# Kernel optimization log

Hardware: AMD Instinct MI355X
Metric: run time of the kernel (lower is better)

## Reference

```python
import jax, jax.numpy as jnp
import numpy as np

K = 4          # deform conv kernel size
STRIDE = 4     # deform conv stride (no padding)
EPS = 1e-5     # BatchNorm eps
SLOPE = 0.01   # LeakyReLU default negative slope


def conv2d(x, w, b, stride):
    out = jax.lax.conv_general_dilated(
        x, w, (stride, stride), 'VALID',
        dimension_numbers=('NCHW', 'OIHW', 'NCHW'))
    return out + b[None, :, None, None]


def batchnorm(x, g, b, m, v):
    inv = g / jnp.sqrt(v + EPS)
    return x * inv[None, :, None, None] + (b - m * inv)[None, :, None, None]


def leaky_relu(x):
    return jnp.where(x >= 0, x, SLOPE * x)


def deform_conv(x, offset, w, b):
    # x: [B,C,H,W], offset: [B,2*K*K,Ho,Wo] with (dy,dx) interleaved per kernel tap
    B, C, H, W = x.shape
    Ho, Wo = offset.shape[2], offset.shape[3]
    KK = K * K
    off = offset.reshape(B, KK, 2, Ho, Wo)
    kh = jnp.repeat(jnp.arange(K), K).astype(x.dtype)   # [KK] kernel row
    kw = jnp.tile(jnp.arange(K), K).astype(x.dtype)     # [KK] kernel col
    base_y = (jnp.arange(Ho) * STRIDE).astype(x.dtype)
    base_x = (jnp.arange(Wo) * STRIDE).astype(x.dtype)
    # sampling coordinates [B,KK,Ho,Wo]
    py = base_y[None, None, :, None] + kh[None, :, None, None] + off[:, :, 0]
    px = base_x[None, None, None, :] + kw[None, :, None, None] + off[:, :, 1]
    y0 = jnp.floor(py)
    x0 = jnp.floor(px)
    wy = py - y0
    wx = px - x0

    def corner(yc, xc):
        yi = yc.astype(jnp.int32)
        xi = xc.astype(jnp.int32)
        valid = (yi >= 0) & (yi < H) & (xi >= 0) & (xi < W)
        yi = jnp.clip(yi, 0, H - 1)
        xi = jnp.clip(xi, 0, W - 1)
        # per-batch gather: [B,C,KK,Ho,Wo]
        v = jax.vmap(lambda img, a, c: img[:, a, c])(x, yi, xi)
        return v * valid[:, None].astype(x.dtype)

    v00 = corner(y0, x0)
    v01 = corner(y0, x0 + 1)
    v10 = corner(y0 + 1, x0)
    v11 = corner(y0 + 1, x0 + 1)
    wy_ = wy[:, None]
    wx_ = wx[:, None]
    sampled = (v00 * (1 - wy_) * (1 - wx_) + v01 * (1 - wy_) * wx_
               + v10 * wy_ * (1 - wx_) + v11 * wy_ * wx_)  # [B,C,KK,Ho,Wo]
    out = jnp.einsum('bckhw,ock->bohw', sampled, w.reshape(w.shape[0], C, KK))
    return out + b[None, :, None, None]


def setup_inputs() -> dict:
    key = jax.random.key(0)
    ks = jax.random.split(key, 16)
    f32 = jnp.float32
    inp = {
        'x': jax.random.normal(ks[0], (64, 3, 224, 224), f32),
        'stem_w': jax.random.normal(ks[1], (96, 3, 4, 4), f32) * 0.1,
        'stem_b': jax.random.normal(ks[2], (96,), f32) * 0.05,
        'bn1_g': jax.random.uniform(ks[3], (96,), f32, 0.5, 1.5),
        'bn1_b': jax.random.normal(ks[4], (96,), f32) * 0.05,
        'bn1_m': jax.random.normal(ks[5], (96,), f32) * 0.05,
        'bn1_v': jax.random.uniform(ks[6], (96,), f32, 0.5, 1.5),
        'off_w': jax.random.normal(ks[7], (32, 96, 4, 4), f32) * 0.02,
        'off_b': jax.random.normal(ks[8], (32,), f32) * 0.02,
        'dcn_w': jax.random.normal(ks[9], (768, 96, 4, 4), f32) * 0.05,
        'dcn_b': jax.random.normal(ks[10], (768,), f32) * 0.05,
        'bn2_g': jax.random.uniform(ks[11], (768,), f32, 0.5, 1.5),
        'bn2_b': jax.random.normal(ks[12], (768,), f32) * 0.05,
        'bn2_m': jax.random.normal(ks[13], (768,), f32) * 0.05,
        'bn2_v': jax.random.uniform(ks[14], (768,), f32, 0.5, 1.5),
    }
    return inp


def reference(x, stem_w, stem_b, bn1_g, bn1_b, bn1_m, bn1_v,
              off_w, off_b, dcn_w, dcn_b, bn2_g, bn2_b, bn2_m, bn2_v):
    h = conv2d(x, stem_w, stem_b, 4)                      # [B,96,56,56]
    h = leaky_relu(batchnorm(h, bn1_g, bn1_b, bn1_m, bn1_v))
    offset = conv2d(h, off_w, off_b, 4)                   # [B,32,14,14]
    h = deform_conv(h, offset, dcn_w, dcn_b)              # [B,768,14,14]
    h = leaky_relu(batchnorm(h, bn2_g, bn2_b, bn2_m, bn2_v))
    B, C, Ho, Wo = h.shape
    return h.reshape(B, C, Ho * Wo).transpose(0, 2, 1)    # [B,196,768]
```

## Files before the change

kernel.cpp:

```cpp
#include <hip/hip_runtime.h>

#define EPS   1e-5f
#define SLOPE 0.01f

#define WS_H1   0L
#define WS_OFF  19267584L
#define WS_W1T  19668992L
#define WS_S1   19673600L
#define WS_T1   19673696L
#define WS_T2   19673792L
#define WS_SB   19674560L
#define WS_H1P  29308352L
#define WS_WTB  38942144L
#define WS_WOB  39531968L

__device__ __forceinline__ unsigned short f2bf(float f) {
    unsigned int u = __builtin_bit_cast(unsigned int, f);
    u += 0x7fffu + ((u >> 16) & 1u);
    return (unsigned short)(u >> 16);
}

typedef __attribute__((ext_vector_type(4))) unsigned short ushort4v;
typedef __attribute__((ext_vector_type(8))) short bf16x8;
typedef __attribute__((ext_vector_type(4))) float floatx4;

__global__ __launch_bounds__(256) void k0_prep(
    const float* __restrict__ stem_w, const float* __restrict__ stem_b,
    const float* __restrict__ bn1_g,  const float* __restrict__ bn1_b,
    const float* __restrict__ bn1_m,  const float* __restrict__ bn1_v,
    const float* __restrict__ off_w,  const float* __restrict__ dcn_w,
    const float* __restrict__ dcn_b,  const float* __restrict__ bn2_g,
    const float* __restrict__ bn2_b,  const float* __restrict__ bn2_m,
    const float* __restrict__ bn2_v,  float* __restrict__ ws)
{
    long i = (long)blockIdx.x * 256 + threadIdx.x;
    unsigned short* Wtb = (unsigned short*)(ws + WS_WTB);
    unsigned short* Wob = (unsigned short*)(ws + WS_WOB);
    if (i < 1179648L) {
        int oc = (int)(i / 1536), k = (int)(i % 1536);
        int kk = k / 96, c = k % 96;
        float inv2 = bn2_g[oc] * rsqrtf(bn2_v[oc] + EPS);
        Wtb[i] = f2bf(dcn_w[oc * 1536 + c * 16 + kk] * inv2);
    } else if (i < 1228800L) {
        int i2 = (int)(i - 1179648L);
        int oc = i2 / 1536, k = i2 % 1536;
        int khw = k / 96, c = k % 96;
        Wob[i2] = f2bf(off_w[oc * 1536 + c * 16 + khw]);
    } else if (i < 1233408L) {
        int i3 = (int)(i - 1228800L);
        int k = i3 / 96, c = i3 % 96;
        ws[WS_W1T + i3] = stem_w[c * 48 + k];
    } else if (i < 1233504L) {
        int c = (int)(i - 1233408L);
        ws[WS_S1 + c] = bn1_g[c] * rsqrtf(bn1_v[c] + EPS);
    } else if (i < 1233600L) {
        int c = (int)(i - 1233504L);
        float s = bn1_g[c] * rsqrtf(bn1_v[c] + EPS);
        ws[WS_T1 + c] = stem_b[c] * s + bn1_b[c] - bn1_m[c] * s;
    } else if (i < 1234368L) {
        int oc = (int)(i - 1233600L);
        float inv2 = bn2_g[oc] * rsqrtf(bn2_v[oc] + EPS);
        ws[WS_T2 + oc] = dcn_b[oc] * inv2 + bn2_b[oc] - bn2_m[oc] * inv2;
    }
}

__global__ __launch_bounds__(256) void k1_stem(
    const float* __restrict__ x, const float* __restrict__ w1t,
    const float* __restrict__ s1, const float* __restrict__ t1,
    float* __restrict__ h1, unsigned short* __restrict__ h1p)
{
    const int oy = blockIdx.x;
    const int b  = blockIdx.y;
    const int tid = threadIdx.x;

    __shared__ float xs[3 * 4 * 224];
    __shared__ float wsh[48 * 100];
    __shared__ float s1s[96], t1s[96];

    for (int i = tid; i < 2688; i += 256) {
        int ci = i / 896, r = i % 896;
        int kh = r / 224, xx = r % 224;
        xs[i] = x[((long)(b * 3 + ci) * 224 + oy * 4 + kh) * 224 + xx];
    }
    for (int i = tid; i < 4608; i += 256) {
        int k = i / 96, c = i % 96;
        wsh[k * 100 + c] = w1t[i];
    }
    if (tid < 96) { s1s[tid] = s1[tid]; t1s[tid] = t1[tid]; }
    __syncthreads();

    for (int u = tid; u < 336; u += 256) {
        int oxg = u / 24, cg = u % 24;
        float acc[4][4] = {};
#pragma unroll
        for (int ci = 0; ci < 3; ci++) {
#pragma unroll
            for (int kh = 0; kh < 4; kh++) {
                const float* xrow = &xs[(ci * 4 + kh) * 224 + oxg * 16];
                float4 xv[4], wv[4];
#pragma unroll
                for (int o = 0; o < 4; o++) xv[o] = *(const float4*)&xrow[o * 4];
#pragma unroll
                for (int kw = 0; kw < 4; kw++)
                    wv[kw] = *(const float4*)&wsh[(ci * 16 + kh * 4 + kw) * 100 + cg * 4];
#pragma unroll
                for (int kw = 0; kw < 4; kw++) {
                    const float* wf = (const float*)&wv[kw];
#pragma unroll
                    for (int o = 0; o < 4; o++) {
                        float xv_s = ((const float*)&xv[o])[kw];
#pragma unroll
                        for (int cc = 0; cc < 4; cc++)
                            acc[o][cc] += xv_s * wf[cc];
                    }
                }
            }
        }
#pragma unroll
        for (int o = 0; o < 4; o++) {
            float4 r;
            float* rp = (float*)&r;
#pragma unroll
            for (int cc = 0; cc < 4; cc++) {
                int c = cg * 4 + cc;
                float v = acc[o][cc] * s1s[c] + t1s[c];
                rp[cc] = v >= 0.f ? v : SLOPE * v;
            }
            *(float4*)&h1[((long)((b * 56 + oy) * 56) + oxg * 4 + o) * 96 + cg * 4] = r;
            ushort4v hp;
            hp.x = f2bf(rp[0]); hp.y = f2bf(rp[1]);
            hp.z = f2bf(rp[2]); hp.w = f2bf(rp[3]);
            long np = ((long)(b * 196 + (oy >> 2) * 14 + oxg) * 16 + (oy & 3) * 4 + o);
            *(ushort4v*)&h1p[np * 96 + cg * 4] = hp;
        }
    }
}

__global__ __launch_bounds__(256) void k2_mfma(
    const unsigned short* __restrict__ A,
    const unsigned short* __restrict__ Wob,
    const float* __restrict__ off_b, float* __restrict__ off)
{
    const int tid  = threadIdx.x;
    const int wave = tid >> 6;
    const int lane = tid & 63;
    const int n0   = blockIdx.x * 128;
    const int m    = lane & 15;
    const int quad = lane >> 4;

    __shared__ unsigned short sA[128 * 32];
    __shared__ unsigned short sB[32 * 32];

    const int srow  = wave * 32 + (lane >> 2);
    const int skoff = (lane & 3) * 8;
    const unsigned short* gA0 = A + (long)(n0 + srow) * 1536 + skoff;
    const unsigned short* gA1 = gA0 + 16L * 1536;
    unsigned short* lA0 = &sA[(wave * 32 +  0) * 32];
    unsigned short* lA1 = &sA[(wave * 32 + 16) * 32];
    const unsigned short* gB = Wob + (long)((wave & 1) * 16 + (lane >> 2)) * 1536 + skoff;
    unsigned short* lB = &sB[((wave & 1) * 16) * 32];

    floatx4 acc[2][2];
#pragma unroll
    for (int i = 0; i < 2; i++)
#pragma unroll
        for (int j = 0; j < 2; j++) acc[i][j] = (floatx4)0.f;

    for (int kt = 0; kt < 48; ++kt) {
        __syncthreads();
        __builtin_amdgcn_global_load_lds(
            (const __attribute__((address_space(1))) void*)gA0,
            (__attribute__((address_space(3))) void*)lA0, 16, 0, 0);
        __builtin_amdgcn_global_load_lds(
            (const __attribute__((address_space(1))) void*)gA1,
            (__attribute__((address_space(3))) void*)lA1, 16, 0, 0);
        if (wave < 2)
            __builtin_amdgcn_global_load_lds(
                (const __attribute__((address_space(1))) void*)gB,
                (__attribute__((address_space(3))) void*)lB, 16, 0, 0);
        gA0 += 32; gA1 += 32; gB += 32;
        __syncthreads();

        bf16x8 af[2], bfr[2];
#pragma unroll
        for (int i = 0; i < 2; i++)
            af[i] = *(const bf16x8*)&sA[(wave * 32 + i * 16 + m) * 32 + quad * 8];
#pragma unroll
        for (int j = 0; j < 2; j++)
            bfr[j] = *(const bf16x8*)&sB[(j * 16 + m) * 32 + quad * 8];
#pragma unroll
        for (int i = 0; i < 2; i++)
#pragma unroll
            for (int j = 0; j < 2; j++)
                acc[i][j] = __builtin_amdgcn_mfma_f32_16x16x32_bf16(
                    af[i], bfr[j], acc[i][j], 0, 0, 0);
    }

    float tb[2];
#pragma unroll
    for (int j = 0; j < 2; j++) tb[j] = off_b[j * 16 + m];
#pragma unroll
    for (int i = 0; i < 2; i++)
#pragma unroll
        for (int r = 0; r < 4; r++) {
            long n = n0 + wave * 32 + i * 16 + quad * 4 + r;
#pragma unroll
            for (int j = 0; j < 2; j++)
                off[n * 32 + j * 16 + m] = acc[i][j][r] + tb[j];
        }
}

__global__ __launch_bounds__(384) void k3_sample(
    const float* __restrict__ h1, const float* __restrict__ off,
    unsigned short* __restrict__ S)
{
    const int p = blockIdx.x;
    const int b = blockIdx.y;
    const int y = p / 14, xo = p % 14;
    const int tid = threadIdx.x;
    const int c4 = tid % 24, kk = tid / 24;
    const int kh = kk >> 2, kw = kk & 3;

    const float* ob = off + ((long)((b * 14 + y) * 14 + xo)) * 32;
    float dy = ob[kk * 2];
    float dx = ob[kk * 2 + 1];

    float py = (float)(y * 4 + kh) + dy;
    float px = (float)(xo * 4 + kw) + dx;
    float y0f = floorf(py), x0f = floorf(px);
    float wy = py - y0f, wx = px - x0f;
    int y0 = (int)y0f, x0 = (int)x0f;
    int y1 = y0 + 1,  x1 = x0 + 1;

    float my0 = (y0 >= 0 && y0 < 56) ? 1.f : 0.f;
    float my1 = (y1 >= 0 && y1 < 56) ? 1.f : 0.f;
    float mx0 = (x0 >= 0 && x0 < 56) ? 1.f : 0.f;
    float mx1 = (x1 >= 0 && x1 < 56) ? 1.f : 0.f;
    int y0c = min(max(y0, 0), 55), y1c = min(max(y1, 0), 55);
    int x0c = min(max(x0, 0), 55), x1c = min(max(x1, 0), 55);

    const float* hb = h1 + (long)b * 56 * 56 * 96 + c4 * 4;
    float4 v00 = *(const float4*)&hb[(y0c * 56 + x0c) * 96];
    float4 v01 = *(const float4*)&hb[(y0c * 56 + x1c) * 96];
    float4 v10 = *(const float4*)&hb[(y1c * 56 + x0c) * 96];
    float4 v11 = *(const float4*)&hb[(y1c * 56 + x1c) * 96];

    float w00 = my0 * mx0 * (1.f - wy) * (1.f - wx);
    float w01 = my0 * mx1 * (1.f - wy) * wx;
    float w10 = my1 * mx0 * wy * (1.f - wx);
    float w11 = my1 * mx1 * wy * wx;

    ushort4v rr;
    rr.x = f2bf(v00.x * w00 + v01.x * w01 + v10.x * w10 + v11.x * w11);
    rr.y = f2bf(v00.y * w00 + v01.y * w01 + v10.y * w10 + v11.y * w11);
    rr.z = f2bf(v00.z * w00 + v01.z * w01 + v10.z * w10 + v11.z * w11);
    rr.w = f2bf(v00.w * w00 + v01.w * w01 + v10.w * w10 + v11.w * w11);

    long n = (long)b * 196 + p;
    *(ushort4v*)&S[n * 1536 + kk * 96 + c4 * 4] = rr;
}

__global__ __launch_bounds__(256) void k4_gemm_mfma(
    const unsigned short* __restrict__ S,
    const unsigned short* __restrict__ Wtb,
    const float* __restrict__ t2, float* __restrict__ out)
{
    const int tid  = threadIdx.x;
    const int wave = tid >> 6;
    const int lane = tid & 63;
    const int oc0 = blockIdx.x * 128;
    const int n0  = blockIdx.y * 128;
    const int wr  = wave >> 1, wc = wave & 1;
    const int m    = lane & 15;
    const int quad = lane >> 4;

    __shared__ unsigned short sA[128 * 32];
    __shared__ unsigned short sB[128 * 32];

    const int srow  = wave * 32 + (lane >> 2);
    const int skoff = (lane & 3) * 8;
    const unsigned short* gA0 = S   + (long)(n0  + srow) * 1536 + skoff;
    const unsigned short* gA1 = gA0 + 16L * 1536;
    const unsigned short* gB0 = Wtb + (long)(oc0 + srow) * 1536 + skoff;
    const unsigned short* gB1 = gB0 + 16L * 1536;
    unsigned short* lA0 = &sA[(wave * 32 +  0) * 32];
    unsigned short* lA1 = &sA[(wave * 32 + 16) * 32];
    unsigned short* lB0 = &sB[(wave * 32 +  0) * 32];
    unsigned short* lB1 = &sB[(wave * 32 + 16) * 32];

    floatx4 acc[4][4];
#pragma unroll
    for (int i = 0; i < 4; i++)
#pragma unroll
        for (int j = 0; j < 4; j++) acc[i][j] = (floatx4)0.f;

    for (int kt = 0; kt < 48; ++kt) {
        __syncthreads();
        __builtin_amdgcn_global_load_lds(
            (const __attribute__((address_space(1))) void*)gA0,
            (__attribute__((address_space(3))) void*)lA0, 16, 0, 0);
        __builtin_amdgcn_global_load_lds(
            (const __attribute__((address_space(1))) void*)gA1,
            (__attribute__((address_space(3))) void*)lA1, 16, 0, 0);
        __builtin_amdgcn_global_load_lds(
            (const __attribute__((address_space(1))) void*)gB0,
            (__attribute__((address_space(3))) void*)lB0, 16, 0, 0);
        __builtin_amdgcn_global_load_lds(
            (const __attribute__((address_space(1))) void*)gB1,
            (__attribute__((address_space(3))) void*)lB1, 16, 0, 0);
        gA0 += 32; gA1 += 32; gB0 += 32; gB1 += 32;
        __syncthreads();

        bf16x8 af[4], bf[4];
#pragma unroll
        for (int i = 0; i < 4; i++)
            af[i] = *(const bf16x8*)&sA[(wr * 64 + i * 16 + m) * 32 + quad * 8];
#pragma unroll
        for (int j = 0; j < 4; j++)
            bf[j] = *(const bf16x8*)&sB[(wc * 64 + j * 16 + m) * 32 + quad * 8];
#pragma unroll
        for (int i = 0; i < 4; i++)
#pragma unroll
            for (int j = 0; j < 4; j++)
                acc[i][j] = __builtin_amdgcn_mfma_f32_16x16x32_bf16(
                    af[i], bf[j], acc[i][j], 0, 0, 0);
    }

    float tb[4];
#pragma unroll
    for (int j = 0; j < 4; j++) tb[j] = t2[oc0 + wc * 64 + j * 16 + m];
#pragma unroll
    for (int i = 0; i < 4; i++) {
#pragma unroll
        for (int r = 0; r < 4; r++) {
            long n = n0 + wr * 64 + i * 16 + quad * 4 + r;
            float* orow = out + n * 768 + oc0 + wc * 64 + m;
#pragma unroll
            for (int j = 0; j < 4; j++) {
                float v = acc[i][j][r] + tb[j];
                orow[j * 16] = v >= 0.f ? v : SLOPE * v;
            }
        }
    }
}

extern "C" void kernel_launch(void* const* d_in, const int* in_sizes, int n_in,
                              void* d_out, int out_size, void* d_ws, size_t ws_size,
                              hipStream_t stream)
{
    const float* x      = (const float*)d_in[0];
    const float* stem_w = (const float*)d_in[1];
    const float* stem_b = (const float*)d_in[2];
    const float* bn1_g  = (const float*)d_in[3];
    const float* bn1_b  = (const float*)d_in[4];
    const float* bn1_m  = (const float*)d_in[5];
    const float* bn1_v  = (const float*)d_in[6];
    const float* off_w  = (const float*)d_in[7];
    const float* off_b  = (const float*)d_in[8];
    const float* dcn_w  = (const float*)d_in[9];
    const float* dcn_b  = (const float*)d_in[10];
    const float* bn2_g  = (const float*)d_in[11];
    const float* bn2_b  = (const float*)d_in[12];
    const float* bn2_m  = (const float*)d_in[13];
    const float* bn2_v  = (const float*)d_in[14];

    float* ws  = (float*)d_ws;
    float* out = (float*)d_out;

    float* h1  = ws + WS_H1;
    float* off = ws + WS_OFF;
    float* w1t = ws + WS_W1T;
    float* s1  = ws + WS_S1;
    float* t1  = ws + WS_T1;
    float* t2  = ws + WS_T2;
    unsigned short* Sb  = (unsigned short*)(ws + WS_SB);
    unsigned short* h1p = (unsigned short*)(ws + WS_H1P);
    unsigned short* Wtb = (unsigned short*)(ws + WS_WTB);
    unsigned short* Wob = (unsigned short*)(ws + WS_WOB);

    k0_prep<<<4823, 256, 0, stream>>>(stem_w, stem_b, bn1_g, bn1_b, bn1_m, bn1_v,
                                      off_w, dcn_w, dcn_b, bn2_g, bn2_b, bn2_m,
                                      bn2_v, ws);
    k1_stem<<<dim3(56, 64), 256, 0, stream>>>(x, w1t, s1, t1, h1, h1p);
    k2_mfma<<<98, 256, 0, stream>>>(h1p, Wob, off_b, off);
    k3_sample<<<dim3(196, 64), 384, 0, stream>>>(h1, off, Sb);
    k4_gemm_mfma<<<dim3(6, 98), 256, 0, stream>>>(Sb, Wtb, t2, out);
}
```

Baseline: 262.4 us.

## Store stem activations once in bf16 and gather patches directly in offset conv

The stem kernel now writes a single bf16 NHWC activation instead of both an fp32 copy and a separate patch-ordered bf16 copy. The offset-conv GEMM computes patch addresses on the fly from the NHWC layout, and the bilinear sampler reads bf16 values, converts them to float and interpolates. The stem block size is raised to 384 so each thread handles one work item without a second loop pass. This cuts stem write traffic and halves sampler gather bytes, at the cost of sampling from bf16-rounded activations and less contiguous loads in the offset GEMM.

After: 252.7 us. -3.7%, faster.

```diff
diff --git a/kernel.cpp b/kernel.cpp
--- a/kernel.cpp
+++ b/kernel.cpp
@@ -3,21 +3,24 @@
 #define EPS   1e-5f
 #define SLOPE 0.01f
 
-#define WS_H1   0L
-#define WS_OFF  19267584L
-#define WS_W1T  19668992L
-#define WS_S1   19673600L
-#define WS_T1   19673696L
-#define WS_T2   19673792L
-#define WS_SB   19674560L
-#define WS_H1P  29308352L
-#define WS_WTB  38942144L
-#define WS_WOB  39531968L
+#define WS_H1B  0L
+#define WS_OFF  9633792L
+#define WS_W1T  10035200L
+#define WS_S1   10039808L
+#define WS_T1   10039904L
+#define WS_T2   10040000L
+#define WS_SB   10040768L
+#define WS_WTB  19674560L
+#define WS_WOB  20264384L
 
 __device__ __forceinline__ unsigned short f2bf(float f) {
     unsigned int u = __builtin_bit_cast(unsigned int, f);
     u += 0x7fffu + ((u >> 16) & 1u);
     return (unsigned short)(u >> 16);
+}
+__device__ __forceinline__ float bf2f(unsigned short u) {
+    unsigned int t = ((unsigned int)u) << 16;
+    return __builtin_bit_cast(float, t);
 }
 
 typedef __attribute__((ext_vector_type(4))) unsigned short ushort4v;
@@ -64,10 +67,10 @@
     }
 }
 
-__global__ __launch_bounds__(256) void k1_stem(
+__global__ __launch_bounds__(384) void k1_stem(
     const float* __restrict__ x, const float* __restrict__ w1t,
     const float* __restrict__ s1, const float* __restrict__ t1,
-    float* __restrict__ h1, unsigned short* __restrict__ h1p)
+    unsigned short* __restrict__ h1)
 {
     const int oy = blockIdx.x;
     const int b  = blockIdx.y;
@@ -77,20 +80,20 @@
     __shared__ float wsh[48 * 100];
     __shared__ float s1s[96], t1s[96];
 
-    for (int i = tid; i < 2688; i += 256) {
+    for (int i = tid; i < 2688; i += 384) {
         int ci = i / 896, r = i % 896;
         int kh = r / 224, xx = r % 224;
         xs[i] = x[((long)(b * 3 + ci) * 224 + oy * 4 + kh) * 224 + xx];
     }
-    for (int i = tid; i < 4608; i += 256) {
+    for (int i = tid; i < 4608; i += 384) {
         int k = i / 96, c = i % 96;
         wsh[k * 100 + c] = w1t[i];
     }
     if (tid < 96) { s1s[tid] = s1[tid]; t1s[tid] = t1[tid]; }
     __syncthreads();
 
-    for (int u = tid; u < 336; u += 256) {
-        int oxg = u / 24, cg = u % 24;
+    if (tid < 336) {
+        int oxg = tid / 24, cg = tid % 24;
         float acc[4][4] = {};
 #pragma unroll
         for (int ci = 0; ci < 3; ci++) {
@@ -118,26 +121,21 @@
         }
 #pragma unroll
         for (int o = 0; o < 4; o++) {
-            float4 r;
-            float* rp = (float*)&r;
+            ushort4v hp;
 #pragma unroll
             for (int cc = 0; cc < 4; cc++) {
                 int c = cg * 4 + cc;
                 float v = acc[o][cc] * s1s[c] + t1s[c];
-                rp[cc] = v >= 0.f ? v : SLOPE * v;
+                v = v >= 0.f ? v : SLOPE * v;
+                ((unsigned short*)&hp)[cc] = f2bf(v);
             }
-            *(float4*)&h1[((long)((b * 56 + oy) * 56) + oxg * 4 + o) * 96 + cg * 4] = r;
-            ushort4v hp;
-            hp.x = f2bf(rp[0]); hp.y = f2bf(rp[1]);
-            hp.z = f2bf(rp[2]); hp.w = f2bf(rp[3]);
-            long np = ((long)(b * 196 + (oy >> 2) * 14 + oxg) * 16 + (oy & 3) * 4 + o);
-            *(ushort4v*)&h1p[np * 96 + cg * 4] = hp;
+            *(ushort4v*)&h1[((long)((b * 56 + oy) * 56) + oxg * 4 + o) * 96 + cg * 4] = hp;
         }
     }
 }
 
 __global__ __launch_bounds__(256) void k2_mfma(
-    const unsigned short* __restrict__ A,
+    const unsigned short* __restrict__ h1,
     const unsigned short* __restrict__ Wob,
     const float* __restrict__ off_b, float* __restrict__ off)
 {
@@ -151,14 +149,18 @@
     __shared__ unsigned short sA[128 * 32];
     __shared__ unsigned short sB[32 * 32];
 
-    const int srow  = wave * 32 + (lane >> 2);
     const int skoff = (lane & 3) * 8;
-    const unsigned short* gA0 = A + (long)(n0 + srow) * 1536 + skoff;
-    const unsigned short* gA1 = gA0 + 16L * 1536;
+    int n_a = n0 + wave * 32 + (lane >> 2);
+    int n_b = n_a + 16;
+    int ba = n_a / 196, pa = n_a % 196;
+    int bb = n_b / 196, pb = n_b % 196;
+    long pixa = ((long)(ba * 56 + (pa / 14) * 4) * 56 + (pa % 14) * 4);
+    long pixb = ((long)(bb * 56 + (pb / 14) * 4) * 56 + (pb % 14) * 4);
+
+    const unsigned short* gB = Wob + (long)((wave & 1) * 16 + (lane >> 2)) * 1536 + skoff;
     unsigned short* lA0 = &sA[(wave * 32 +  0) * 32];
     unsigned short* lA1 = &sA[(wave * 32 + 16) * 32];
-    const unsigned short* gB = Wob + (long)((wave & 1) * 16 + (lane >> 2)) * 1536 + skoff;
-    unsigned short* lB = &sB[((wave & 1) * 16) * 32];
+    unsigned short* lB  = &sB[((wave & 1) * 16) * 32];
 
     floatx4 acc[2][2];
 #pragma unroll
@@ -167,6 +169,13 @@
         for (int j = 0; j < 2; j++) acc[i][j] = (floatx4)0.f;
 
     for (int kt = 0; kt < 48; ++kt) {
+        int khw = kt / 3;
+        int c0  = (kt - khw * 3) * 32;
+        int kh  = khw >> 2, kw = khw & 3;
+        long eoff = (long)(kh * 56 + kw) * 96 + c0 + skoff;
+        const unsigned short* gA0 = h1 + pixa * 96 + eoff;
+        const unsigned short* gA1 = h1 + pixb * 96 + eoff;
+
         __syncthreads();
         __builtin_amdgcn_global_load_lds(
             (const __attribute__((address_space(1))) void*)gA0,
@@ -178,7 +187,7 @@
             __builtin_amdgcn_global_load_lds(
                 (const __attribute__((address_space(1))) void*)gB,
                 (__attribute__((address_space(3))) void*)lB, 16, 0, 0);
-        gA0 += 32; gA1 += 32; gB += 32;
+        gB += 32;
         __syncthreads();
 
         bf16x8 af[2], bfr[2];
@@ -211,7 +220,7 @@
 }
 
 __global__ __launch_bounds__(384) void k3_sample(
-    const float* __restrict__ h1, const float* __restrict__ off,
+    const unsigned short* __restrict__ h1, const float* __restrict__ off,
     unsigned short* __restrict__ S)
 {
     const int p = blockIdx.x;
@@ -221,7 +230,7 @@
     const int c4 = tid % 24, kk = tid / 24;
     const int kh = kk >> 2, kw = kk & 3;
 
-    const float* ob = off + ((long)((b * 14 + y) * 14 + xo)) * 32;
+    const float* ob = off + ((long)(b * 196 + p)) * 32;
     float dy = ob[kk * 2];
     float dx = ob[kk * 2 + 1];
 
@@ -239,11 +248,11 @@
     int y0c = min(max(y0, 0), 55), y1c = min(max(y1, 0), 55);
     int x0c = min(max(x0, 0), 55), x1c = min(max(x1, 0), 55);
 
-    const float* hb = h1 + (long)b * 56 * 56 * 96 + c4 * 4;
-    float4 v00 = *(const float4*)&hb[(y0c * 56 + x0c) * 96];
-    float4 v01 = *(const float4*)&hb[(y0c * 56 + x1c) * 96];
-    float4 v10 = *(const float4*)&hb[(y1c * 56 + x0c) * 96];
-    float4 v11 = *(const float4*)&hb[(y1c * 56 + x1c) * 96];
+    const unsigned short* hb = h1 + (long)b * 56 * 56 * 96 + c4 * 4;
+    ushort4v v00 = *(const ushort4v*)&hb[(y0c * 56 + x0c) * 96];
+    ushort4v v01 = *(const ushort4v*)&hb[(y0c * 56 + x1c) * 96];
+    ushort4v v10 = *(const ushort4v*)&hb[(y1c * 56 + x0c) * 96];
+    ushort4v v11 = *(const ushort4v*)&hb[(y1c * 56 + x1c) * 96];
 
     float w00 = my0 * mx0 * (1.f - wy) * (1.f - wx);
     float w01 = my0 * mx1 * (1.f - wy) * wx;
@@ -251,10 +260,14 @@
     float w11 = my1 * mx1 * wy * wx;
 
     ushort4v rr;
-    rr.x = f2bf(v00.x * w00 + v01.x * w01 + v10.x * w10 + v11.x * w11);
-    rr.y = f2bf(v00.y * w00 + v01.y * w01 + v10.y * w10 + v11.y * w11);
-    rr.z = f2bf(v00.z * w00 + v01.z * w01 + v10.z * w10 + v11.z * w11);
-    rr.w = f2bf(v00.w * w00 + v01.w * w01 + v10.w * w10 + v11.w * w11);
+#pragma unroll
+    for (int c = 0; c < 4; c++) {
+        float v = bf2f(((unsigned short*)&v00)[c]) * w00
+                + bf2f(((unsigned short*)&v01)[c]) * w01
+                + bf2f(((unsigned short*)&v10)[c]) * w10
+                + bf2f(((unsigned short*)&v11)[c]) * w11;
+        ((unsigned short*)&rr)[c] = f2bf(v);
+    }
 
     long n = (long)b * 196 + p;
     *(ushort4v*)&S[n * 1536 + kk * 96 + c4 * 4] = rr;
@@ -367,22 +380,21 @@
     float* ws  = (float*)d_ws;
     float* out = (float*)d_out;
 
-    float* h1  = ws + WS_H1;
+    unsigned short* h1  = (unsigned short*)(ws + WS_H1B);
     float* off = ws + WS_OFF;
     float* w1t = ws + WS_W1T;
     float* s1  = ws + WS_S1;
     float* t1  = ws + WS_T1;
     float* t2  = ws + WS_T2;
     unsigned short* Sb  = (unsigned short*)(ws + WS_SB);
-    unsigned short* h1p = (unsigned short*)(ws + WS_H1P);
     unsigned short* Wtb = (unsigned short*)(ws + WS_WTB);
     unsigned short* Wob = (unsigned short*)(ws + WS_WOB);
 
     k0_prep<<<4823, 256, 0, stream>>>(stem_w, stem_b, bn1_g, bn1_b, bn1_m, bn1_v,
                                       off_w, dcn_w, dcn_b, bn2_g, bn2_b, bn2_m,
                                       bn2_v, ws);
-    k1_stem<<<dim3(56, 64), 256, 0, stream>>>(x, w1t, s1, t1, h1, h1p);
-    k2_mfma<<<98, 256, 0, stream>>>(h1p, Wob, off_b, off);
+    k1_stem<<<dim3(56, 64), 384, 0, stream>>>(x, w1t, s1, t1, h1);
+    k2_mfma<<<98, 256, 0, stream>>>(h1, Wob, off_b, off);
     k3_sample<<<dim3(196, 64), 384, 0, stream>>>(h1, off, Sb);
     k4_gemm_mfma<<<dim3(6, 98), 256, 0, stream>>>(Sb, Wtb, t2, out);
 }
```
